# Kernel optimization log

Hardware: AMD Instinct MI355X
Metric: run time of the kernel (lower is better)

Reference implementation:

```python
import jax, jax.numpy as jnp
import numpy as np

B, N, DIM = 32, 3136, 64
H, DH, AGENTS = 8, 8, 49
INNER = H * DH  # 64
SCALE = DH ** -0.5


def setup_inputs() -> dict:
    key = jax.random.key(0)
    ks = jax.random.split(key, 7)
    s = 0.05
    return {
        "x1": jax.random.normal(ks[0], (B, N, DIM), jnp.float32),
        "x2": jax.random.normal(ks[1], (B, N, INNER), jnp.float32),
        "Wq": jax.random.normal(ks[2], (INNER, DIM), jnp.float32) * s,   # to_q (out,in)
        "Wk": jax.random.normal(ks[3], (DIM, INNER), jnp.float32) * s,   # to_k
        "Wv": jax.random.normal(ks[4], (DIM, INNER), jnp.float32) * s,   # to_v
        "Wo": jax.random.normal(ks[5], (2 * DIM, 2 * DIM), jnp.float32) * s,  # to_out linear
        "bo": jax.random.normal(ks[6], (2 * DIM,), jnp.float32) * s,
    }


def _split_heads(t):
    # (b, n, h*d) -> (b, h, n, d)
    b, n, hd = t.shape
    return t.reshape(b, n, H, hd // H).transpose(0, 2, 1, 3)


def reference(x1, x2, Wq, Wk, Wv, Wo, bo):
    b, n, _ = x1.shape
    q = x1 @ Wq.T                      # (b, n, 64)
    k = x2 @ Wk.T                      # (b, n, dim=64)
    v = x2 @ Wv.T
    # AdaptiveAvgPool2d((49, dim)): n % 49 == 0 and channel 64->64 is identity,
    # so pooling is an exact block mean over the sequence axis.
    agent = q.reshape(b, AGENTS, n // AGENTS, q.shape[-1]).mean(axis=2)  # (b, 49, 64)

    agent_h = _split_heads(agent)      # (b, h, 49, d)
    q1 = _split_heads(q)               # (b, h, n, d)
    k_h = _split_heads(k)
    v_h = _split_heads(v)

    # stage 0: agent tokens attend over keys/values (dropout is identity at eval)
    dots0 = jnp.einsum('bhid,bhjd->bhij', agent_h, k_h) * SCALE   # (b,h,49,n)
    attn0 = jax.nn.softmax(dots0, axis=-1)
    out0 = jnp.einsum('bhij,bhjd->bhid', attn0, v_h)              # (b,h,49,d)

    # stage 1: queries attend over agent tokens
    dots1 = jnp.einsum('bhid,bhjd->bhij', q1, agent_h) * SCALE    # (b,h,n,49)
    attn1 = jax.nn.softmax(dots1, axis=-1)
    out1 = jnp.einsum('bhij,bhjd->bhid', attn1, out0)             # (b,h,n,d)

    out1 = out1.transpose(0, 2, 1, 3).reshape(b, n, -1)           # (b,n,64)
    out1 = jnp.concatenate([out1, x1], axis=-1)                   # (b,n,128)
    return out1 @ Wo.T + bo
```

## Files before the change

### kernel.cpp

```cpp
#include <hip/hip_runtime.h>
#include <hip/hip_bf16.h>

#define NB 32
#define NSEQ 3136
#define NDIM 64
#define NH 8
#define NAG 49
#define SPLIT 4

static constexpr float kScale = 0.35355339059327378f;
static constexpr float kLog2e = 1.4426950408889634f;

typedef unsigned short us;
typedef __attribute__((ext_vector_type(8))) __bf16 bf16x8;
typedef __attribute__((ext_vector_type(2))) _Float16 f16x2;
typedef __attribute__((ext_vector_type(4))) _Float16 f16x4;
typedef __attribute__((ext_vector_type(8))) _Float16 f16x8;
typedef __attribute__((ext_vector_type(4))) float f32x4;
typedef __attribute__((ext_vector_type(2))) float f32x2;

__device__ __forceinline__ float fexp2(float x) {
#if __has_builtin(__builtin_amdgcn_exp2f)
  return __builtin_amdgcn_exp2f(x);
#else
  return exp2f(x);
#endif
}

__device__ __forceinline__ float frcp(float x) {
#if __has_builtin(__builtin_amdgcn_rcpf)
  return __builtin_amdgcn_rcpf(x);
#else
  return 1.f / x;
#endif
}

__device__ __forceinline__ unsigned pk2(float a, float b) {
#if __has_builtin(__builtin_amdgcn_cvt_pkrtz)
  return __builtin_bit_cast(unsigned, __builtin_amdgcn_cvt_pkrtz(a, b));
#else
  f16x2 v = {(_Float16)a, (_Float16)b};
  return __builtin_bit_cast(unsigned, v);
#endif
}

__device__ __forceinline__ f16x2 bch(unsigned u) { return __builtin_bit_cast(f16x2, u); }

__global__ __launch_bounds__(256) void prep_kernel(
    const float* __restrict__ Wq, const float* __restrict__ Wk,
    const float* __restrict__ Wv, const float* __restrict__ Wo,
    __bf16* __restrict__ wq, __bf16* __restrict__ wk, __bf16* __restrict__ wv,
    __bf16* __restrict__ wo, us* __restrict__ kvhk, us* __restrict__ vt) {
  int i = blockIdx.x * 256 + threadIdx.x;
  wo[i] = (__bf16)Wo[i];
  if (i < 4096) { wq[i] = (__bf16)Wq[i]; wk[i] = (__bf16)Wk[i]; wv[i] = (__bf16)Wv[i]; }
  if (i < 32) kvhk[(size_t)NB * NH * NSEQ * 8 + i] = 0;
  const us one = 0x3C00;
  for (size_t j = i; j < (size_t)NB * NH * NSEQ; j += 16384) {
    size_t bh = j / NSEQ, tok = j - bh * NSEQ;
    vt[(bh * 9 + 8) * NSEQ + tok] = one;
  }
}

__global__ __launch_bounds__(256, 4) void qkv_agent_kernel(
    const float* __restrict__ x1, const float* __restrict__ x2,
    const float* __restrict__ Wq, const __bf16* __restrict__ wk,
    const __bf16* __restrict__ wv, us* __restrict__ kvhk, us* __restrict__ vt,
    us* __restrict__ agf16) {
  __shared__ __align__(16) __bf16 xb[64][72];
  __shared__ __align__(16) float red[4][64];
  __shared__ __align__(16) float marr[64];
  const int a = blockIdx.x, b = blockIdx.y, t = threadIdx.x;
  const int i64 = t & 63, cb = t >> 6;
  const int w = cb, lr = (t >> 4) & 3, lc = t & 15;

  bf16x8 ak0 = *(const bf16x8*)(wk + (size_t)(w * 16 + lc) * NDIM + lr * 8);
  bf16x8 ak1 = *(const bf16x8*)(wk + (size_t)(w * 16 + lc) * NDIM + 32 + lr * 8);
  bf16x8 av0 = *(const bf16x8*)(wv + (size_t)(w * 16 + lc) * NDIM + lr * 8);
  bf16x8 av1 = *(const bf16x8*)(wv + (size_t)(w * 16 + lc) * NDIM + 32 + lr * 8);

  {
    const float4* s2 = (const float4*)(x2 + ((size_t)(b * NSEQ) + a * 64 + i64) * NDIM + cb * 16);
    float4 v0 = s2[0], v1 = s2[1], v2 = s2[2], v3 = s2[3];
    bf16x8 p0, p1;
    p0[0]=(__bf16)v0.x; p0[1]=(__bf16)v0.y; p0[2]=(__bf16)v0.z; p0[3]=(__bf16)v0.w;
    p0[4]=(__bf16)v1.x; p0[5]=(__bf16)v1.y; p0[6]=(__bf16)v1.z; p0[7]=(__bf16)v1.w;
    p1[0]=(__bf16)v2.x; p1[1]=(__bf16)v2.y; p1[2]=(__bf16)v2.z; p1[3]=(__bf16)v2.w;
    p1[4]=(__bf16)v3.x; p1[5]=(__bf16)v3.y; p1[6]=(__bf16)v3.z; p1[7]=(__bf16)v3.w;
    *(bf16x8*)&xb[i64][cb * 16] = p0; *(bf16x8*)&xb[i64][cb * 16 + 8] = p1;
  }
  {
    const float* xc = x1 + ((size_t)(b * NSEQ) + a * 64 + cb * 16) * NDIM + i64;
    float cs = 0.f;
#pragma unroll
    for (int i = 0; i < 16; ++i) cs += xc[i * NDIM];
    red[cb][i64] = cs;
  }
  __syncthreads();

  f32x4 acck[4], accv[4];
#pragma unroll
  for (int i = 0; i < 4; ++i) {
    acck[i] = (f32x4){0.f, 0.f, 0.f, 0.f};
    accv[i] = (f32x4){0.f, 0.f, 0.f, 0.f};
  }
#pragma unroll
  for (int nt = 0; nt < 4; ++nt) {
    bf16x8 x0 = *(const bf16x8*)&xb[nt * 16 + lc][lr * 8];
    bf16x8 x1f = *(const bf16x8*)&xb[nt * 16 + lc][32 + lr * 8];
    acck[nt] = __builtin_amdgcn_mfma_f32_16x16x32_bf16(ak0, x0, acck[nt], 0, 0, 0);
    acck[nt] = __builtin_amdgcn_mfma_f32_16x16x32_bf16(ak1, x1f, acck[nt], 0, 0, 0);
    accv[nt] = __builtin_amdgcn_mfma_f32_16x16x32_bf16(av0, x0, accv[nt], 0, 0, 0);
    accv[nt] = __builtin_amdgcn_mfma_f32_16x16x32_bf16(av1, x1f, accv[nt], 0, 0, 0);
  }
  const int head = 2 * w + (lr >> 1), sb = (lr & 1) * 4;
  {
    _Float16* kdst = (_Float16*)kvhk + ((size_t)(b * NH + head) * NSEQ) * 8 + sb;
#pragma unroll
    for (int nt = 0; nt < 4; ++nt) {
      const int tok = a * 64 + nt * 16 + lc;
      f16x4 pk4;
      pk4[0]=(_Float16)acck[nt][0]; pk4[1]=(_Float16)acck[nt][1];
      pk4[2]=(_Float16)acck[nt][2]; pk4[3]=(_Float16)acck[nt][3];
      *(f16x4*)(kdst + (size_t)tok * 8) = pk4;
    }
  }
  __syncthreads();

  _Float16 (*vtile)[72] = (_Float16(*)[72])xb;
  {
    const int f0 = w * 16 + lr * 4;
#pragma unroll
    for (int nt = 0; nt < 4; ++nt) {
      const int tok = nt * 16 + lc;
#pragma unroll
      for (int j = 0; j < 4; ++j) vtile[f0 + j][tok] = (_Float16)accv[nt][j];
    }
  }
  if (t < 64) marr[t] = red[0][t] + red[1][t] + red[2][t] + red[3][t];
  __syncthreads();

  {
    const int r = t >> 2, p = t & 3;
    _Float16* drow = (_Float16*)vt +
        ((size_t)(b * NH + (r >> 3)) * 9 + (r & 7)) * NSEQ + a * 64 + p * 16;
    f16x8 v0 = *(const f16x8*)&vtile[r][p * 16];
    f16x8 v1 = *(const f16x8*)&vtile[r][p * 16 + 8];
    *(f16x8*)drow = v0;
    *(f16x8*)(drow + 8) = v1;
  }
  if (t < 64) {
    const float4* wqr = (const float4*)(Wq + (size_t)t * NDIM);
    const float4* mm = (const float4*)marr;
    float s0 = 0.f;
#pragma unroll
    for (int i = 0; i < 16; ++i) {
      float4 wv4 = wqr[i], m4 = mm[i];
      s0 += wv4.x * m4.x + wv4.y * m4.y + wv4.z * m4.z + wv4.w * m4.w;
    }
    const float val = s0 * (kScale * kLog2e / 64.f);
    ((_Float16*)agf16)[(((size_t)b * NH + (t >> 3)) * NAG + a) * 8 + (t & 7)] =
        (_Float16)val;
  }
}

__global__ __launch_bounds__(256, 4) void stage0_kernel(
    const us* __restrict__ kvhk, const us* __restrict__ vt,
    const us* __restrict__ agf16, float* __restrict__ pvs_z) {
  __shared__ _Float16 pshuf[4][4][16][40];
  __shared__ float redS[64][12];
  const int h = blockIdx.x, b = blockIdx.y, z = blockIdx.z;
  const int t = threadIdx.x, l = t & 63, w = t >> 6;
  for (int i = t; i < 64 * 12; i += 256) (&redS[0][0])[i] = 0.f;

  const int lg = l >> 4, lm = l & 15;
  const size_t bh = (size_t)b * NH + h;
  const us* kb = kvhk + bh * ((size_t)NSEQ * 8);
  const us* vb = vt + bh * ((size_t)9 * NSEQ);
  const us* ab = agf16 + bh * (NAG * 8);

  f16x8 ba[4];
#pragma unroll
  for (int at = 0; at < 4; ++at) {
    f16x8 v = (f16x8)(_Float16)0.0f;
    if (lg == 0) {
      int row = at * 16 + lm; if (row > 48) row = 48;
      v = *(const f16x8*)(ab + row * 8);
    }
    ba[at] = v;
  }
  const us* vrow = vb + (size_t)((lm > 8) ? 8 : lm) * NSEQ + lg * 8;

  f32x4 accPV[4];
#pragma unroll
  for (int i = 0; i < 4; ++i) accPV[i] = (f32x4){0.f, 0.f, 0.f, 0.f};

  _Float16* ps = &pshuf[w][0][0][0];
  const int iw = z * 4 + w;
  __syncthreads();

  f16x8 aK0, aK1, bV;
  aK0 = *(const f16x8*)(kb + ((size_t)iw * 32 + lm) * 8 + lg * 8);
  aK1 = *(const f16x8*)(kb + ((size_t)iw * 32 + 16 + lm) * 8 + lg * 8);
  bV  = *(const f16x8*)(vrow + iw * 32);

  for (int c = iw; c < 98; c += 16) {
    f16x8 nK0, nK1, nV;
    const int cn = c + 16;
    if (cn < 98) {
      nK0 = *(const f16x8*)(kb + ((size_t)cn * 32 + lm) * 8 + lg * 8);
      nK1 = *(const f16x8*)(kb + ((size_t)cn * 32 + 16 + lm) * 8 + lg * 8);
      nV  = *(const f16x8*)(vrow + cn * 32);
    }
#pragma unroll
    for (int at = 0; at < 4; ++at) {
      f32x4 s0 = __builtin_amdgcn_mfma_f32_16x16x32_f16(
          aK0, ba[at], (f32x4){0.f, 0.f, 0.f, 0.f}, 0, 0, 0);
      f32x4 s1 = __builtin_amdgcn_mfma_f32_16x16x32_f16(
          aK1, ba[at], (f32x4){0.f, 0.f, 0.f, 0.f}, 0, 0, 0);
      unsigned p00 = pk2(fexp2(s0[0]), fexp2(s0[1]));
      unsigned p01 = pk2(fexp2(s0[2]), fexp2(s0[3]));
      unsigned p10 = pk2(fexp2(s1[0]), fexp2(s1[1]));
      unsigned p11 = pk2(fexp2(s1[2]), fexp2(s1[3]));
      unsigned long long q0 = ((unsigned long long)p01 << 32) | p00;
      unsigned long long q1 = ((unsigned long long)p11 << 32) | p10;
      _Float16* prow = ps + (size_t)(at * 16 + lm) * 40;
      *(unsigned long long*)(prow + lg * 4) = q0;
      *(unsigned long long*)(prow + 16 + lg * 4) = q1;
    }
#pragma unroll
    for (int at = 0; at < 4; ++at) {
      f16x8 aP = *(const f16x8*)(ps + (size_t)(at * 16 + lm) * 40 + lg * 8);
      accPV[at] = __builtin_amdgcn_mfma_f32_16x16x32_f16(aP, bV, accPV[at], 0, 0, 0);
    }
    aK0 = nK0; aK1 = nK1; bV = nV;
  }

  if (lm < 9) {
#pragma unroll
    for (int at = 0; at < 4; ++at)
#pragma unroll
      for (int jj = 0; jj < 4; ++jj) {
        const int ag = at * 16 + lg * 4 + jj;
        if (ag < NAG) atomicAdd(&redS[ag][lm], accPV[at][jj]);
      }
  }
  __syncthreads();
  float* pz = pvs_z + ((size_t)z * (NB * NH) + bh) * (NAG * 12);
  for (int i = t; i < NAG * 9; i += 256) {
    pz[(i / 9) * 12 + (i % 9)] = redS[i / 9][i % 9];
  }
}

__global__ __launch_bounds__(64) void aofin_kernel(
    const us* __restrict__ agf16, const float* __restrict__ pvs_z,
    us* __restrict__ aof16) {
  const int h = blockIdx.x, b = blockIdx.y, t = threadIdx.x;
  if (t >= NAG) return;
  const size_t bh = (size_t)b * NH + h;
  f32x4 pv0 = (f32x4){0.f,0.f,0.f,0.f}, pv1 = (f32x4){0.f,0.f,0.f,0.f};
  float den = 0.f;
#pragma unroll
  for (int zz = 0; zz < SPLIT; ++zz) {
    const float* pp = pvs_z + (((size_t)zz * (NB * NH) + bh) * NAG + t) * 12;
    pv0 += *(const f32x4*)pp;
    pv1 += *(const f32x4*)(pp + 4);
    den += pp[8];
  }
  float inv = frcp(den);
  pv0 *= inv; pv1 *= inv;
  us* dst = aof16 + (bh * NAG + t) * 16;
  *(uint4*)dst = *(const uint4*)(agf16 + (bh * NAG + t) * 8);
  f16x4 a, c;
  a[0]=(_Float16)pv0[0]; a[1]=(_Float16)pv0[1]; a[2]=(_Float16)pv0[2]; a[3]=(_Float16)pv0[3];
  c[0]=(_Float16)pv1[0]; c[1]=(_Float16)pv1[1]; c[2]=(_Float16)pv1[2]; c[3]=(_Float16)pv1[3];
  *(f16x4*)(dst + 8) = a;
  *(f16x4*)(dst + 12) = c;
}

__global__ __launch_bounds__(512, 8) void stage1_out_kernel(
    const float* __restrict__ x1, const __bf16* __restrict__ wq,
    const us* __restrict__ aof16, const __bf16* __restrict__ wo,
    const float* __restrict__ bo, float* __restrict__ out) {
  __shared__ __align__(16) __bf16 xa[64][72];
  __shared__ __align__(16) us qcat[64][72];
  __shared__ __align__(16) us aof[392 * 16];
  const int tile = blockIdx.x, b = blockIdx.y;
  const int t = threadIdx.x, tokl = t & 63, h = t >> 6;
  const int w = h, lr = (t >> 4) & 3, lc = t & 15;
  const int mtile = w & 3, thalf = w >> 2;

  bf16x8 wqf0 = *(const bf16x8*)(wq + (size_t)(mtile * 16 + lc) * NDIM + lr * 8);
  bf16x8 wqf1 = *(const bf16x8*)(wq + (size_t)(mtile * 16 + lc) * NDIM + 32 + lr * 8);

  {
    const float4* src = (const float4*)(x1 + ((size_t)b * NSEQ + tile * 64 + tokl) * NDIM + h * 8);
    float4 v0 = src[0], v1 = src[1];
    bf16x8 p;
    p[0]=(__bf16)v0.x; p[1]=(__bf16)v0.y; p[2]=(__bf16)v0.z; p[3]=(__bf16)v0.w;
    p[4]=(__bf16)v1.x; p[5]=(__bf16)v1.y; p[6]=(__bf16)v1.z; p[7]=(__bf16)v1.w;
    *(bf16x8*)&xa[tokl][h * 8] = p;
  }
  {
    const uint4* src = (const uint4*)(aof16 + (size_t)b * (NH * NAG * 16));
    uint4* dst = (uint4*)aof;
    for (int i = t; i < 784; i += 512) dst[i] = src[i];
  }
  __syncthreads();

  {
    f32x4 aq[2];
    aq[0] = (f32x4){0.f,0.f,0.f,0.f}; aq[1] = (f32x4){0.f,0.f,0.f,0.f};
#pragma unroll
    for (int nt = 0; nt < 2; ++nt) {
      bf16x8 bx0 = *(const bf16x8*)&xa[thalf * 32 + nt * 16 + lc][lr * 8];
      bf16x8 bx1 = *(const bf16x8*)&xa[thalf * 32 + nt * 16 + lc][32 + lr * 8];
      aq[nt] = __builtin_amdgcn_mfma_f32_16x16x32_bf16(wqf0, bx0, aq[nt], 0, 0, 0);
      aq[nt] = __builtin_amdgcn_mfma_f32_16x16x32_bf16(wqf1, bx1, aq[nt], 0, 0, 0);
    }
#pragma unroll
    for (int nt = 0; nt < 2; ++nt) {
      f16x4 pk;
      pk[0]=(_Float16)aq[nt][0]; pk[1]=(_Float16)aq[nt][1];
      pk[2]=(_Float16)aq[nt][2]; pk[3]=(_Float16)aq[nt][3];
      *(f16x4*)&qcat[thalf * 32 + nt * 16 + lc][mtile * 16 + lr * 4] = pk;
    }
  }
  __syncthreads();

  {
    uint4 qv = *(const uint4*)&qcat[tokl][h * 8];
    f16x2 q0 = bch(qv.x), q1 = bch(qv.y), q2 = bch(qv.z), q3 = bch(qv.w);
    const us* hrow = aof + (h * NAG) * 16;
    float s = 0.f;
    f16x2 o01 = (f16x2)(_Float16)0.f, o23 = o01, o45 = o01, o67 = o01;
#pragma unroll 7
    for (int a2 = 0; a2 < NAG; ++a2) {
      const us* r = hrow + a2 * 16;
      uint4 A = *(const uint4*)r;
      uint4 V = *(const uint4*)(r + 8);
      float lg;
#if __has_builtin(__builtin_amdgcn_fdot2)
      lg = __builtin_amdgcn_fdot2(q0, bch(A.x), 0.f, false);
      lg = __builtin_amdgcn_fdot2(q1, bch(A.y), lg, false);
      lg = __builtin_amdgcn_fdot2(q2, bch(A.z), lg, false);
      lg = __builtin_amdgcn_fdot2(q3, bch(A.w), lg, false);
#else
      f16x2 a0 = bch(A.x), a1 = bch(A.y), a2_ = bch(A.z), a3 = bch(A.w);
      lg = (float)q0[0]*(float)a0[0] + (float)q0[1]*(float)a0[1]
         + (float)q1[0]*(float)a1[0] + (float)q1[1]*(float)a1[1]
         + (float)q2[0]*(float)a2_[0] + (float)q2[1]*(float)a2_[1]
         + (float)q3[0]*(float)a3[0] + (float)q3[1]*(float)a3[1];
#endif
      float p = fexp2(lg);
      s += p;
      _Float16 pf = (_Float16)p;
      f16x2 pp = {pf, pf};
      o01 += pp * bch(V.x); o23 += pp * bch(V.y);
      o45 += pp * bch(V.z); o67 += pp * bch(V.w);
    }
    float inv = frcp(s);
    bf16x8 pc;
    pc[0]=(__bf16)((float)o01[0]*inv); pc[1]=(__bf16)((float)o01[1]*inv);
    pc[2]=(__bf16)((float)o23[0]*inv); pc[3]=(__bf16)((float)o23[1]*inv);
    pc[4]=(__bf16)((float)o45[0]*inv); pc[5]=(__bf16)((float)o45[1]*inv);
    pc[6]=(__bf16)((float)o67[0]*inv); pc[7]=(__bf16)((float)o67[1]*inv);
    *(bf16x8*)&qcat[tokl][h * 8] = pc;
  }
  bf16x8 wof[4];
#pragma unroll
  for (int ks = 0; ks < 4; ++ks)
    wof[ks] = *(const bf16x8*)(wo + (size_t)(w * 16 + lc) * 128 + ks * 32 + lr * 8);
  f32x4 bv = *(const f32x4*)(bo + w * 16 + lr * 4);
  __syncthreads();

  {
    f32x4 acc[4];
#pragma unroll
    for (int i = 0; i < 4; ++i) acc[i] = (f32x4){0.f,0.f,0.f,0.f};
#pragma unroll
    for (int ks = 0; ks < 4; ++ks) {
#pragma unroll
      for (int nt = 0; nt < 4; ++nt) {
        bf16x8 bx = (ks < 2) ? *(const bf16x8*)&qcat[nt * 16 + lc][ks * 32 + lr * 8]
                             : *(const bf16x8*)&xa[nt * 16 + lc][(ks - 2) * 32 + lr * 8];
        acc[nt] = __builtin_amdgcn_mfma_f32_16x16x32_bf16(wof[ks], bx, acc[nt], 0, 0, 0);
      }
    }
#pragma unroll
    for (int nt = 0; nt < 4; ++nt) {
      f32x4 v = acc[nt] + bv;
      float* dst = out + ((size_t)b * NSEQ + tile * 64 + nt * 16 + lc) * 128 + w * 16 + lr * 4;
      *(f32x4*)dst = v;
    }
  }
}

extern "C" void kernel_launch(void* const* d_in, const int* in_sizes, int n_in,
                              void* d_out, int out_size, void* d_ws, size_t ws_size,
                              hipStream_t stream) {
  (void)in_sizes; (void)n_in; (void)out_size; (void)ws_size;
  const float* x1 = (const float*)d_in[0];
  const float* x2 = (const float*)d_in[1];
  const float* Wq = (const float*)d_in[2];
  const float* Wk = (const float*)d_in[3];
  const float* Wv = (const float*)d_in[4];
  const float* Wo = (const float*)d_in[5];
  const float* bo = (const float*)d_in[6];
  float* out = (float*)d_out;

  us* vt = (us*)d_ws;
  us* kvhk = vt + (size_t)NB * NH * 9 * NSEQ;
  us* agf16 = kvhk + (size_t)NB * NH * NSEQ * 8 + 32;
  float* pvs_z = (float*)(agf16 + (size_t)NB * NH * NAG * 8);
  us* aof16 = (us*)(pvs_z + (size_t)SPLIT * NB * NH * NAG * 12);
  __bf16* wq_bf = (__bf16*)(aof16 + (size_t)NB * NH * NAG * 16);
  __bf16* wk_bf = wq_bf + 4096;
  __bf16* wv_bf = wk_bf + 4096;
  __bf16* wo_bf = wv_bf + 4096;

  prep_kernel<<<dim3(64), 256, 0, stream>>>(Wq, Wk, Wv, Wo, wq_bf, wk_bf, wv_bf,
                                            wo_bf, kvhk, vt);
  qkv_agent_kernel<<<dim3(NAG, NB), 256, 0, stream>>>(x1, x2, Wq, wk_bf, wv_bf,
                                                      kvhk, vt, agf16);
  stage0_kernel<<<dim3(NH, NB, SPLIT), 256, 0, stream>>>(kvhk, vt, agf16, pvs_z);
  aofin_kernel<<<dim3(NH, NB), 64, 0, stream>>>(agf16, pvs_z, aof16);
  stage1_out_kernel<<<dim3(NAG, NB), 512, 0, stream>>>(x1, wq_bf, aof16, wo_bf,
                                                       bo, out);
}
```

Before: 79.69 us.

## Compute stage-1 agent attention with f16 MFMA instead of scalar fdot2 loop

```diff
diff --git a/kernel.cpp b/kernel.cpp
--- a/kernel.cpp
+++ b/kernel.cpp
@@ -43,8 +43,6 @@
   return __builtin_bit_cast(unsigned, v);
 #endif
 }
-
-__device__ __forceinline__ f16x2 bch(unsigned u) { return __builtin_bit_cast(f16x2, u); }
 
 __global__ __launch_bounds__(256) void prep_kernel(
     const float* __restrict__ Wq, const float* __restrict__ Wk,
@@ -253,45 +251,65 @@
 }
 
 __global__ __launch_bounds__(64) void aofin_kernel(
-    const us* __restrict__ agf16, const float* __restrict__ pvs_z,
-    us* __restrict__ aof16) {
+    const float* __restrict__ pvs_z, us* __restrict__ pvtF) {
   const int h = blockIdx.x, b = blockIdx.y, t = threadIdx.x;
-  if (t >= NAG) return;
   const size_t bh = (size_t)b * NH + h;
   f32x4 pv0 = (f32x4){0.f,0.f,0.f,0.f}, pv1 = (f32x4){0.f,0.f,0.f,0.f};
   float den = 0.f;
-#pragma unroll
-  for (int zz = 0; zz < SPLIT; ++zz) {
-    const float* pp = pvs_z + (((size_t)zz * (NB * NH) + bh) * NAG + t) * 12;
-    pv0 += *(const f32x4*)pp;
-    pv1 += *(const f32x4*)(pp + 4);
-    den += pp[8];
-  }
-  float inv = frcp(den);
-  pv0 *= inv; pv1 *= inv;
-  us* dst = aof16 + (bh * NAG + t) * 16;
-  *(uint4*)dst = *(const uint4*)(agf16 + (bh * NAG + t) * 8);
-  f16x4 a, c;
-  a[0]=(_Float16)pv0[0]; a[1]=(_Float16)pv0[1]; a[2]=(_Float16)pv0[2]; a[3]=(_Float16)pv0[3];
-  c[0]=(_Float16)pv1[0]; c[1]=(_Float16)pv1[1]; c[2]=(_Float16)pv1[2]; c[3]=(_Float16)pv1[3];
-  *(f16x4*)(dst + 8) = a;
-  *(f16x4*)(dst + 12) = c;
-}
-
-__global__ __launch_bounds__(512, 8) void stage1_out_kernel(
+  if (t < NAG) {
+#pragma unroll
+    for (int zz = 0; zz < SPLIT; ++zz) {
+      const float* pp = pvs_z + (((size_t)zz * (NB * NH) + bh) * NAG + t) * 12;
+      pv0 += *(const f32x4*)pp;
+      pv1 += *(const f32x4*)(pp + 4);
+      den += pp[8];
+    }
+  }
+  float inv = (t < NAG) ? frcp(den) : 0.f;
+  us* col = pvtF + bh * 1024 + t;
+  _Float16 v0 = (_Float16)(pv0[0]*inv), v1 = (_Float16)(pv0[1]*inv);
+  _Float16 v2 = (_Float16)(pv0[2]*inv), v3 = (_Float16)(pv0[3]*inv);
+  _Float16 v4 = (_Float16)(pv1[0]*inv), v5 = (_Float16)(pv1[1]*inv);
+  _Float16 v6 = (_Float16)(pv1[2]*inv), v7 = (_Float16)(pv1[3]*inv);
+  col[0*64] = __builtin_bit_cast(us, v0); col[1*64] = __builtin_bit_cast(us, v1);
+  col[2*64] = __builtin_bit_cast(us, v2); col[3*64] = __builtin_bit_cast(us, v3);
+  col[4*64] = __builtin_bit_cast(us, v4); col[5*64] = __builtin_bit_cast(us, v5);
+  col[6*64] = __builtin_bit_cast(us, v6); col[7*64] = __builtin_bit_cast(us, v7);
+  col[8*64] = (t < NAG) ? (us)0x3C00 : (us)0;
+#pragma unroll
+  for (int f = 9; f < 16; ++f) col[f*64] = 0;
+}
+
+__global__ __launch_bounds__(512, 6) void stage1_out_kernel(
     const float* __restrict__ x1, const __bf16* __restrict__ wq,
-    const us* __restrict__ aof16, const __bf16* __restrict__ wo,
-    const float* __restrict__ bo, float* __restrict__ out) {
+    const us* __restrict__ agf16, const us* __restrict__ pvtF,
+    const __bf16* __restrict__ wo, const float* __restrict__ bo,
+    float* __restrict__ out) {
   __shared__ __align__(16) __bf16 xa[64][72];
   __shared__ __align__(16) us qcat[64][72];
-  __shared__ __align__(16) us aof[392 * 16];
+  __shared__ __align__(16) _Float16 pW[8][16][72];
   const int tile = blockIdx.x, b = blockIdx.y;
   const int t = threadIdx.x, tokl = t & 63, h = t >> 6;
-  const int w = h, lr = (t >> 4) & 3, lc = t & 15;
+  const int w = h, lane = t & 63, lr = (lane >> 4) & 3, lc = lane & 15;
   const int mtile = w & 3, thalf = w >> 2;
+  const size_t bh = (size_t)b * NH + w;
 
   bf16x8 wqf0 = *(const bf16x8*)(wq + (size_t)(mtile * 16 + lc) * NDIM + lr * 8);
   bf16x8 wqf1 = *(const bf16x8*)(wq + (size_t)(mtile * 16 + lc) * NDIM + 32 + lr * 8);
+
+  f16x8 ba[4];
+#pragma unroll
+  for (int at = 0; at < 4; ++at) {
+    f16x8 v = (f16x8)(_Float16)0.0f;
+    if (lr == 0) {
+      int row = at * 16 + lc; if (row > 48) row = 48;
+      v = *(const f16x8*)(agf16 + bh * (NAG * 8) + row * 8);
+    }
+    ba[at] = v;
+  }
+  const us* pvb = pvtF + bh * 1024;
+  f16x8 pvB0 = *(const f16x8*)(pvb + lc * 64 + lr * 8);
+  f16x8 pvB1 = *(const f16x8*)(pvb + lc * 64 + 32 + lr * 8);
 
   {
     const float4* src = (const float4*)(x1 + ((size_t)b * NSEQ + tile * 64 + tokl) * NDIM + h * 8);
@@ -301,11 +319,6 @@
     p[4]=(__bf16)v1.x; p[5]=(__bf16)v1.y; p[6]=(__bf16)v1.z; p[7]=(__bf16)v1.w;
     *(bf16x8*)&xa[tokl][h * 8] = p;
   }
-  {
-    const uint4* src = (const uint4*)(aof16 + (size_t)b * (NH * NAG * 16));
-    uint4* dst = (uint4*)aof;
-    for (int i = t; i < 784; i += 512) dst[i] = src[i];
-  }
   __syncthreads();
 
   {
@@ -329,43 +342,34 @@
   __syncthreads();
 
   {
-    uint4 qv = *(const uint4*)&qcat[tokl][h * 8];
-    f16x2 q0 = bch(qv.x), q1 = bch(qv.y), q2 = bch(qv.z), q3 = bch(qv.w);
-    const us* hrow = aof + (h * NAG) * 16;
-    float s = 0.f;
-    f16x2 o01 = (f16x2)(_Float16)0.f, o23 = o01, o45 = o01, o67 = o01;
-#pragma unroll 7
-    for (int a2 = 0; a2 < NAG; ++a2) {
-      const us* r = hrow + a2 * 16;
-      uint4 A = *(const uint4*)r;
-      uint4 V = *(const uint4*)(r + 8);
-      float lg;
-#if __has_builtin(__builtin_amdgcn_fdot2)
-      lg = __builtin_amdgcn_fdot2(q0, bch(A.x), 0.f, false);
-      lg = __builtin_amdgcn_fdot2(q1, bch(A.y), lg, false);
-      lg = __builtin_amdgcn_fdot2(q2, bch(A.z), lg, false);
-      lg = __builtin_amdgcn_fdot2(q3, bch(A.w), lg, false);
-#else
-      f16x2 a0 = bch(A.x), a1 = bch(A.y), a2_ = bch(A.z), a3 = bch(A.w);
-      lg = (float)q0[0]*(float)a0[0] + (float)q0[1]*(float)a0[1]
-         + (float)q1[0]*(float)a1[0] + (float)q1[1]*(float)a1[1]
-         + (float)q2[0]*(float)a2_[0] + (float)q2[1]*(float)a2_[1]
-         + (float)q3[0]*(float)a3[0] + (float)q3[1]*(float)a3[1];
-#endif
-      float p = fexp2(lg);
-      s += p;
-      _Float16 pf = (_Float16)p;
-      f16x2 pp = {pf, pf};
-      o01 += pp * bch(V.x); o23 += pp * bch(V.y);
-      o45 += pp * bch(V.z); o67 += pp * bch(V.w);
-    }
-    float inv = frcp(s);
-    bf16x8 pc;
-    pc[0]=(__bf16)((float)o01[0]*inv); pc[1]=(__bf16)((float)o01[1]*inv);
-    pc[2]=(__bf16)((float)o23[0]*inv); pc[3]=(__bf16)((float)o23[1]*inv);
-    pc[4]=(__bf16)((float)o45[0]*inv); pc[5]=(__bf16)((float)o45[1]*inv);
-    pc[6]=(__bf16)((float)o67[0]*inv); pc[7]=(__bf16)((float)o67[1]*inv);
-    *(bf16x8*)&qcat[tokl][h * 8] = pc;
+    _Float16* psw = &pW[w][0][0];
+    const int swz = (lc & 7) << 4;
+#pragma unroll 1
+    for (int g = 0; g < 4; ++g) {
+      f16x8 qf = *(const f16x8*)&qcat[g * 16 + lc][w * 8];
+#pragma unroll
+      for (int at = 0; at < 4; ++at) {
+        f32x4 sc = __builtin_amdgcn_mfma_f32_16x16x32_f16(
+            ba[at], qf, (f32x4){0.f, 0.f, 0.f, 0.f}, 0, 0, 0);
+        unsigned u0 = pk2(fexp2(sc[0]), fexp2(sc[1]));
+        unsigned u1 = pk2(fexp2(sc[2]), fexp2(sc[3]));
+        unsigned long long q = ((unsigned long long)u1 << 32) | u0;
+        *(unsigned long long*)((char*)psw + lc * 144 + (((at * 32) | (lr * 8)) ^ swz)) = q;
+      }
+      f16x8 pA0 = *(const f16x8*)((char*)psw + lc * 144 + ((lr * 16) ^ swz));
+      f16x8 pA1 = *(const f16x8*)((char*)psw + lc * 144 + ((64 + lr * 16) ^ swz));
+      f32x4 pv = __builtin_amdgcn_mfma_f32_16x16x32_f16(pA0, pvB0,
+                   (f32x4){0.f, 0.f, 0.f, 0.f}, 0, 0, 0);
+      pv = __builtin_amdgcn_mfma_f32_16x16x32_f16(pA1, pvB1, pv, 0, 0, 0);
+#pragma unroll
+      for (int j = 0; j < 4; ++j) {
+        float den = __shfl(pv[j], (lane & 48) | 8);
+        if (lc < 8) {
+          float val = pv[j] * frcp(den);
+          *(__bf16*)&qcat[g * 16 + lr * 4 + j][w * 8 + lc] = (__bf16)val;
+        }
+      }
+    }
   }
   bf16x8 wof[4];
 #pragma unroll
@@ -413,8 +417,8 @@
   us* kvhk = vt + (size_t)NB * NH * 9 * NSEQ;
   us* agf16 = kvhk + (size_t)NB * NH * NSEQ * 8 + 32;
   float* pvs_z = (float*)(agf16 + (size_t)NB * NH * NAG * 8);
-  us* aof16 = (us*)(pvs_z + (size_t)SPLIT * NB * NH * NAG * 12);
-  __bf16* wq_bf = (__bf16*)(aof16 + (size_t)NB * NH * NAG * 16);
+  us* pvtF = (us*)(pvs_z + (size_t)SPLIT * NB * NH * NAG * 12);
+  __bf16* wq_bf = (__bf16*)(pvtF + (size_t)NB * NH * 1024);
   __bf16* wk_bf = wq_bf + 4096;
   __bf16* wv_bf = wk_bf + 4096;
   __bf16* wo_bf = wv_bf + 4096;
@@ -424,7 +428,7 @@
   qkv_agent_kernel<<<dim3(NAG, NB), 256, 0, stream>>>(x1, x2, Wq, wk_bf, wv_bf,
                                                       kvhk, vt, agf16);
   stage0_kernel<<<dim3(NH, NB, SPLIT), 256, 0, stream>>>(kvhk, vt, agf16, pvs_z);
-  aofin_kernel<<<dim3(NH, NB), 64, 0, stream>>>(agf16, pvs_z, aof16);
-  stage1_out_kernel<<<dim3(NAG, NB), 512, 0, stream>>>(x1, wq_bf, aof16, wo_bf,
-                                                       bo, out);
-}
+  aofin_kernel<<<dim3(NH, NB), 64, 0, stream>>>(pvs_z, pvtF);
+  stage1_out_kernel<<<dim3(NAG, NB), 512, 0, stream>>>(x1, wq_bf, agf16, pvtF,
+                                                       wo_bf, bo, out);
+}
```

Result: no change. 79.48 us (-0.3%).
